# Kernel optimization log

Measured on AMD Instinct MI355X. Metric: run time of the kernel, lower is better.

The kernel has to match this reference:

```python
import jax, jax.numpy as jnp
import numpy as np

C_M = 256
C_Z = 128
L = 1024


def setup_inputs() -> dict:
    key = jax.random.key(0)
    ks = jax.random.split(key, 8)
    sequence = jax.random.randint(ks[0], (L,), 0, 21)
    residue_index = jnp.arange(L, dtype=jnp.int64) if jax.config.jax_enable_x64 else jnp.arange(L, dtype=jnp.int32)
    # Linear params (torch Linear: y = x @ W.T + b); store as [in, out] for einsum
    W_msa = jax.random.normal(ks[1], (21, C_M), dtype=jnp.float32) * 0.02
    b_msa = jnp.zeros((C_M,), dtype=jnp.float32)
    W_left = jax.random.normal(ks[2], (21, C_Z), dtype=jnp.float32) * 0.02
    b_left = jnp.zeros((C_Z,), dtype=jnp.float32)
    W_right = jax.random.normal(ks[3], (21, C_Z), dtype=jnp.float32) * 0.02
    b_right = jnp.zeros((C_Z,), dtype=jnp.float32)
    relpos_emb = jax.random.normal(ks[4], (65, C_Z), dtype=jnp.float32) * 0.02
    return {
        "sequence": sequence,
        "residue_index": residue_index,
        "W_msa": W_msa, "b_msa": b_msa,
        "W_left": W_left, "b_left": b_left,
        "W_right": W_right, "b_right": b_right,
        "relpos_emb": relpos_emb,
    }


def reference(sequence, residue_index, W_msa, b_msa, W_left, b_left, W_right, b_right, relpos_emb):
    seq = jnp.clip(sequence, 0, 20)
    # one-hot + Linear == row gather of W plus bias; use one_hot matmul to match math exactly
    one_hot = jax.nn.one_hot(seq, 21, dtype=W_msa.dtype)  # [L, 21]
    msa = (one_hot @ W_msa + b_msa)[None]                  # [1, L, c_m]
    left = one_hot @ W_left + b_left                       # [L, c_z]
    right = one_hot @ W_right + b_right                    # [L, c_z]
    d = jnp.clip(residue_index[:, None] - residue_index[None, :] + 32, 0, 64)  # [L, L]
    pair = left[:, None, :] + right[None, :, :] + relpos_emb[d]                # [L, L, c_z]
    return msa, pair
```

## Files before the change

kernel.cpp:

```cpp
#include <hip/hip_runtime.h>

#define L_SEQ 1024
#define CM    256
#define CZ    128
#define NAA   21
#define NPAIR (NAA * NAA)
#define ROWB  (CZ * 4)
#define TBL_BYTES (3 * NPAIR * ROWB)

typedef float f32x4 __attribute__((ext_vector_type(4)));

static __device__ __forceinline__ int clip21(int s) {
    return s < 0 ? 0 : (s > 20 ? 20 : s);
}

__global__ __launch_bounds__(128) void build_tables(
    const int*   __restrict__ seq,
    const float* __restrict__ Wl,  const float* __restrict__ bl,
    const float* __restrict__ Wr,  const float* __restrict__ br,
    const float* __restrict__ rel,
    float* __restrict__ ws)
{
    const int bx = blockIdx.x;
    const int si = bx / NAA;
    const int sj = bx - si * NAA;
    const int c  = threadIdx.x;
    (void)seq;
    const float cmb = (Wl[si * CZ + c] + bl[c]) + (Wr[sj * CZ + c] + br[c]);
    ws[bx * CZ + c]                 = cmb;
    ws[NPAIR * CZ + bx * CZ + c]    = cmb + rel[c];
    ws[2 * NPAIR * CZ + bx * CZ + c] = cmb + rel[64 * CZ + c];
}

__global__ __launch_bounds__(256, 6) void stream_pair(
    const int*   __restrict__ seq,
    const int*   __restrict__ ri,
    const float* __restrict__ Wm,  const float* __restrict__ bm,
    const float* __restrict__ rel,
    const float* __restrict__ ws,
    float* __restrict__ out_msa,
    float* __restrict__ out_pair)
{
    __shared__ unsigned sd[512];
    const int tid = threadIdx.x;
    const int bx  = blockIdx.x;
    const int i   = bx >> 1;
    const int j0  = (bx & 1) * 512;

    const int s_i  = clip21(seq[i]);
    const int rii  = ri[i];
    const int si21 = s_i * NAA;

    for (int jj = tid; jj < 512; jj += 256) {
        const int j  = j0 + jj;
        const int sj = clip21(seq[j]);
        int d = rii - ri[j] + 32;
        d = d < 0 ? 0 : (d > 64 ? 64 : d);
        const unsigned pr = (unsigned)(si21 + sj);
        sd[jj] = (d == 0)  ? (NPAIR + pr) * ROWB
               : (d == 64) ? (2u * NPAIR + pr) * ROWB
               : (0x80000000u | pr | ((unsigned)d << 9));
    }
    __syncthreads();

    if ((bx & 1) == 0)
        out_msa[i * CM + tid] = Wm[s_i * CM + tid] + bm[tid];

    const int cl = tid & 31;
    const int jo = tid >> 5;
    const int cb = cl * 16;
    const char* wsb  = (const char*)ws;
    const char* relb = (const char*)rel;

    char* outp = (char*)(out_pair + ((size_t)i * L_SEQ + j0 + jo) * CZ) + cb;

    #pragma unroll 8
    for (int it = 0; it < 64; ++it) {
        const unsigned p = sd[it * 8 + jo];
        f32x4 v;
        if (!(p & 0x80000000u)) {
            v = *(const f32x4*)(wsb + p + cb);
        } else {
            const f32x4 a = *(const f32x4*)(wsb + (p & 0x1FFu) * ROWB + cb);
            const f32x4 r = *(const f32x4*)(relb + ((p >> 9) & 0x7Fu) * ROWB + cb);
            v = a + r;
        }
        __builtin_nontemporal_store(v, (f32x4*)outp);
        outp += 8 * ROWB;
    }
}

__global__ __launch_bounds__(256, 4) void fallback_kernel(
    const int*   __restrict__ seq,
    const int*   __restrict__ ri,
    const float* __restrict__ Wm,  const float* __restrict__ bm,
    const float* __restrict__ Wl,  const float* __restrict__ bl,
    const float* __restrict__ Wr,  const float* __restrict__ br,
    const float* __restrict__ rel,
    float* __restrict__ out_msa,
    float* __restrict__ out_pair)
{
    __shared__ float comb   [NAA * CZ];
    __shared__ float comb_lo[NAA * CZ];
    __shared__ float comb_hi[NAA * CZ];
    __shared__ unsigned int sd[512];

    const int tid = threadIdx.x;
    const int bx  = blockIdx.x;
    const int i   = bx >> 1;
    const int j0  = (bx & 1) * 512;

    const int s_i = clip21(seq[i]);
    const int rii = ri[i];

    for (int jj = tid; jj < 512; jj += 256) {
        const int j = j0 + jj;
        const int sj = clip21(seq[j]);
        int d = rii - ri[j] + 32;
        d = d < 0 ? 0 : (d > 64 ? 64 : d);
        sd[jj] = (unsigned)(sj * 512) | ((unsigned)(d * 512) << 16);
    }
    for (int idx = tid; idx < NAA * CZ; idx += 256) {
        const int c = idx & (CZ - 1);
        const float cmb = (Wl[s_i * CZ + c] + bl[c]) + (Wr[idx] + br[c]);
        comb[idx]    = cmb;
        comb_lo[idx] = cmb + rel[c];
        comb_hi[idx] = cmb + rel[64 * CZ + c];
    }
    __syncthreads();

    if ((bx & 1) == 0)
        out_msa[i * CM + tid] = Wm[s_i * CM + tid] + bm[tid];

    const int cb = (tid & 31) * 16;
    const int jo = tid >> 5;
    const char* rel_b     = (const char*)rel;
    const char* comb_b    = (const char*)comb;
    const char* comb_lo_b = (const char*)comb_lo;
    const char* comb_hi_b = (const char*)comb_hi;
    const int lo_thresh = i + 32;
    const int hi_thresh = i - 32 - 7;

    float* outp = out_pair + ((size_t)i * L_SEQ + j0 + jo) * CZ + (cb >> 2);

    #pragma unroll 4
    for (int it = 0; it < 64; ++it) {
        const int jg = j0 + it * 8;
        const unsigned int p   = sd[it * 8 + jo];
        const unsigned int row = p & 0xFFFFu;
        const bool is_lo = (jg >= lo_thresh);
        const bool is_hi = (jg <= hi_thresh);
        const char* base = is_lo ? comb_lo_b : (is_hi ? comb_hi_b : comb_b);
        float4 v = *(const float4*)(base + row + cb);
        if (!(is_lo || is_hi)) {
            const float4 rv = *(const float4*)(rel_b + (p >> 16) + cb);
            v.x += rv.x; v.y += rv.y; v.z += rv.z; v.w += rv.w;
        }
        *(float4*)outp = v;
        outp += 8 * CZ;
    }
}

extern "C" void kernel_launch(void* const* d_in, const int* in_sizes, int n_in,
                              void* d_out, int out_size, void* d_ws, size_t ws_size,
                              hipStream_t stream) {
    const int*   seq = (const int*)d_in[0];
    const int*   ri  = (const int*)d_in[1];
    const float* Wm  = (const float*)d_in[2];
    const float* bm  = (const float*)d_in[3];
    const float* Wl  = (const float*)d_in[4];
    const float* bl  = (const float*)d_in[5];
    const float* Wr  = (const float*)d_in[6];
    const float* br  = (const float*)d_in[7];
    const float* rel = (const float*)d_in[8];

    float* out      = (float*)d_out;
    float* out_msa  = out;
    float* out_pair = out + (size_t)L_SEQ * CM;

    if (ws_size >= (size_t)TBL_BYTES) {
        float* ws = (float*)d_ws;
        hipLaunchKernelGGL(build_tables, dim3(NPAIR), dim3(CZ), 0, stream,
                           seq, Wl, bl, Wr, br, rel, ws);
        hipLaunchKernelGGL(stream_pair, dim3(L_SEQ * 2), dim3(256), 0, stream,
                           seq, ri, Wm, bm, rel, ws, out_msa, out_pair);
    } else {
        hipLaunchKernelGGL(fallback_kernel, dim3(L_SEQ * 2), dim3(256), 0, stream,
                           seq, ri, Wm, bm, Wl, bl, Wr, br, rel, out_msa, out_pair);
    }
}
```

Baseline: 112.7 us.

## Split pair stream into small tiles, drop LDS staging, separate MSA blocks

The pair kernel now launches 16 tiles of 64 columns per row instead of 2 tiles of 512, and each thread computes its own table offset inline rather than staging it through shared memory behind a barrier. The MSA rows move to 32 dedicated blocks at the end of the grid, nontemporal stores become regular stores, and the occupancy hint is raised. The goal is more parallelism with less per-block setup and no sync, at the cost of many more blocks, repeated per-element reads of seq/ri, and losing the streaming-store hint on the 512MB output.

Result: faster. 108.4 us (-3.7%).

```diff
diff --git a/kernel.cpp b/kernel.cpp
--- a/kernel.cpp
+++ b/kernel.cpp
@@ -7,6 +7,8 @@
 #define NPAIR (NAA * NAA)
 #define ROWB  (CZ * 4)
 #define TBL_BYTES (3 * NPAIR * ROWB)
+#define PAIR_TILES (L_SEQ * 16)
+#define MSA_TILES  32
 
 typedef float f32x4 __attribute__((ext_vector_type(4)));
 
@@ -15,7 +17,6 @@
 }
 
 __global__ __launch_bounds__(128) void build_tables(
-    const int*   __restrict__ seq,
     const float* __restrict__ Wl,  const float* __restrict__ bl,
     const float* __restrict__ Wr,  const float* __restrict__ br,
     const float* __restrict__ rel,
@@ -25,14 +26,13 @@
     const int si = bx / NAA;
     const int sj = bx - si * NAA;
     const int c  = threadIdx.x;
-    (void)seq;
     const float cmb = (Wl[si * CZ + c] + bl[c]) + (Wr[sj * CZ + c] + br[c]);
-    ws[bx * CZ + c]                 = cmb;
-    ws[NPAIR * CZ + bx * CZ + c]    = cmb + rel[c];
+    ws[bx * CZ + c]                  = cmb;
+    ws[NPAIR * CZ + bx * CZ + c]     = cmb + rel[c];
     ws[2 * NPAIR * CZ + bx * CZ + c] = cmb + rel[64 * CZ + c];
 }
 
-__global__ __launch_bounds__(256, 6) void stream_pair(
+__global__ __launch_bounds__(256, 8) void stream_pair(
     const int*   __restrict__ seq,
     const int*   __restrict__ ri,
     const float* __restrict__ Wm,  const float* __restrict__ bm,
@@ -41,52 +41,55 @@
     float* __restrict__ out_msa,
     float* __restrict__ out_pair)
 {
-    __shared__ unsigned sd[512];
     const int tid = threadIdx.x;
     const int bx  = blockIdx.x;
-    const int i   = bx >> 1;
-    const int j0  = (bx & 1) * 512;
 
-    const int s_i  = clip21(seq[i]);
-    const int rii  = ri[i];
-    const int si21 = s_i * NAA;
+    if (bx < PAIR_TILES) {
+        const int i  = bx >> 4;
+        const int j0 = (bx & 15) * 64;
 
-    for (int jj = tid; jj < 512; jj += 256) {
-        const int j  = j0 + jj;
-        const int sj = clip21(seq[j]);
-        int d = rii - ri[j] + 32;
-        d = d < 0 ? 0 : (d > 64 ? 64 : d);
-        const unsigned pr = (unsigned)(si21 + sj);
-        sd[jj] = (d == 0)  ? (NPAIR + pr) * ROWB
-               : (d == 64) ? (2u * NPAIR + pr) * ROWB
-               : (0x80000000u | pr | ((unsigned)d << 9));
-    }
-    __syncthreads();
+        const int si21 = clip21(seq[i]) * NAA;
+        const int rii  = ri[i];
 
-    if ((bx & 1) == 0)
-        out_msa[i * CM + tid] = Wm[s_i * CM + tid] + bm[tid];
+        const int cl = tid & 31;
+        const int jo = tid >> 5;
+        const int cb = cl * 16;
+        const char* wsb  = (const char*)ws;
+        const char* relb = (const char*)rel;
 
-    const int cl = tid & 31;
-    const int jo = tid >> 5;
-    const int cb = cl * 16;
-    const char* wsb  = (const char*)ws;
-    const char* relb = (const char*)rel;
+        char* outp = (char*)out_pair + ((size_t)i * L_SEQ + j0 + jo) * ROWB + cb;
 
-    char* outp = (char*)(out_pair + ((size_t)i * L_SEQ + j0 + jo) * CZ) + cb;
+        #pragma unroll 8
+        for (int p = 0; p < 8; ++p) {
+            const int j  = j0 + p * 8 + jo;
+            const int sj = clip21(seq[j]);
+            int d = rii - ri[j] + 32;
+            d = d < 0 ? 0 : (d > 64 ? 64 : d);
+            const unsigned pr = (unsigned)(si21 + sj);
 
-    #pragma unroll 8
-    for (int it = 0; it < 64; ++it) {
-        const unsigned p = sd[it * 8 + jo];
-        f32x4 v;
-        if (!(p & 0x80000000u)) {
-            v = *(const f32x4*)(wsb + p + cb);
-        } else {
-            const f32x4 a = *(const f32x4*)(wsb + (p & 0x1FFu) * ROWB + cb);
-            const f32x4 r = *(const f32x4*)(relb + ((p >> 9) & 0x7Fu) * ROWB + cb);
-            v = a + r;
+            const unsigned off = (d == 0)  ? (NPAIR + pr) * ROWB
+                               : (d == 64) ? (2u * NPAIR + pr) * ROWB
+                                           : pr * ROWB;
+            f32x4 v = *(const f32x4*)(wsb + off + cb);
+            if (d != 0 && d != 64) {
+                const f32x4 r = *(const f32x4*)(relb + (unsigned)d * ROWB + cb);
+                v = v + r;
+            }
+            *(f32x4*)outp = v;
+            outp += 8 * ROWB;
         }
-        __builtin_nontemporal_store(v, (f32x4*)outp);
-        outp += 8 * ROWB;
+    } else {
+        const int m = bx - PAIR_TILES;
+        #pragma unroll 8
+        for (int p = 0; p < 8; ++p) {
+            const int e   = m * 8192 + p * 1024 + tid * 4;
+            const int row = e >> 8;
+            const int col = e & 255;
+            const int s   = clip21(seq[row]);
+            const f32x4 w = *(const f32x4*)(Wm + s * CM + col);
+            const f32x4 b = *(const f32x4*)(bm + col);
+            *(f32x4*)(out_msa + e) = w + b;
+        }
     }
 }
 
@@ -181,8 +184,8 @@
     if (ws_size >= (size_t)TBL_BYTES) {
         float* ws = (float*)d_ws;
         hipLaunchKernelGGL(build_tables, dim3(NPAIR), dim3(CZ), 0, stream,
-                           seq, Wl, bl, Wr, br, rel, ws);
-        hipLaunchKernelGGL(stream_pair, dim3(L_SEQ * 2), dim3(256), 0, stream,
+                           Wl, bl, Wr, br, rel, ws);
+        hipLaunchKernelGGL(stream_pair, dim3(PAIR_TILES + MSA_TILES), dim3(256), 0, stream,
                            seq, ri, Wm, bm, rel, ws, out_msa, out_pair);
     } else {
         hipLaunchKernelGGL(fallback_kernel, dim3(L_SEQ * 2), dim3(256), 0, stream,
```
